# Kernel tuning notes

Measured on AMD Instinct MI355X. Metric: run time of the kernel, lower is better.

The kernel has to match this reference:

```python
import jax, jax.numpy as jnp
import numpy as np

C_M, C_Z, C_H = 256, 128, 32
N_SEQ, N_RES = 128, 256
EPS = 1e-3


def setup_inputs() -> dict:
    key = jax.random.key(0)
    ks = jax.random.split(key, 8)
    s = 0.02
    return {
        "m": jax.random.normal(ks[0], (N_SEQ, N_RES, C_M), dtype=jnp.float32),
        "mask": jnp.ones((N_SEQ, N_RES), dtype=jnp.float32),
        "ln_gamma": jnp.ones((C_M,), dtype=jnp.float32),
        "ln_beta": jnp.zeros((C_M,), dtype=jnp.float32),
        "W1": jax.random.normal(ks[1], (C_M, C_H), dtype=jnp.float32) * s,
        "b1": jnp.zeros((C_H,), dtype=jnp.float32),
        "W2": jax.random.normal(ks[2], (C_M, C_H), dtype=jnp.float32) * s,
        "b2": jnp.zeros((C_H,), dtype=jnp.float32),
        "Wout": jax.random.normal(ks[3], (C_H * C_H, C_Z), dtype=jnp.float32) * s,
        "bout": jnp.zeros((C_Z,), dtype=jnp.float32),
    }


def reference(m, mask, ln_gamma, ln_beta, W1, b1, W2, b2, Wout, bout):
    # LayerNorm over last dim (c_m)
    mu = jnp.mean(m, axis=-1, keepdims=True)
    var = jnp.var(m, axis=-1, keepdims=True)
    ln = (m - mu) * jax.lax.rsqrt(var + 1e-5) * ln_gamma + ln_beta

    mk = mask[..., None]                       # [S, R, 1]
    a = (ln @ W1 + b1) * mk                    # [S, R, c_h]
    b = (ln @ W2 + b2) * mk                    # [S, R, c_h]

    # outer-product mean: contract over the MSA seq dim
    outer = jnp.einsum('sbc,sde->bdce', a, b)  # [R, R, c_h, c_h]
    outer = outer.reshape(N_RES, N_RES, C_H * C_H)
    outer = outer @ Wout + bout                # [R, R, c_z]

    norm = jnp.einsum('sb,sd->bd', mask, mask)[..., None] + EPS  # [R, R, 1]
    return outer / norm
```

## Files before the change

kernel.cpp:

```cpp
#include <hip/hip_runtime.h>

#define S_DIM 128
#define R_DIM 256
#define CM 256
#define CH 32
#define CZ 128

typedef short bf16x8 __attribute__((ext_vector_type(8)));
typedef float f32x4 __attribute__((ext_vector_type(4)));
typedef unsigned short ushort_t;

static __device__ __forceinline__ unsigned short f2bf(float f) {
  union { float f; unsigned u; } v; v.f = f;
  unsigned r = v.u + 0x7FFF + ((v.u >> 16) & 1);
  return (unsigned short)(r >> 16);
}
static __device__ __forceinline__ float bf2f(unsigned short b) {
  union { unsigned u; float f; } v; v.u = ((unsigned)b) << 16;
  return v.f;
}

static __device__ __forceinline__ void gload_lds16(const void* g, void* l) {
  __builtin_amdgcn_global_load_lds(
      (const __attribute__((address_space(1))) void*)g,
      (__attribute__((address_space(3))) void*)l, 16, 0, 0);
}

__global__ __launch_bounds__(256) void prep_kernel(
    const float* __restrict__ W1, const float* __restrict__ b1,
    const float* __restrict__ W2, const float* __restrict__ b2,
    const float* __restrict__ gamma, const float* __restrict__ beta,
    ushort_t* __restrict__ pwT, float* __restrict__ SGCB) {
  int c = blockIdx.x;
  int cm = threadIdx.x;
  __shared__ float red[8];
  float w = (c < 32) ? W1[cm * 32 + c] : W2[cm * 32 + (c - 32)];
  unsigned short pw = f2bf(gamma[cm] * w);
  pwT[c * 256 + cm] = pw;
  float sg = bf2f(pw), cb = beta[cm] * w;
  for (int o = 32; o > 0; o >>= 1) {
    sg += __shfl_down(sg, o);
    cb += __shfl_down(cb, o);
  }
  if ((cm & 63) == 0) { red[cm >> 6] = sg; red[4 + (cm >> 6)] = cb; }
  __syncthreads();
  if (cm == 0) {
    float s = red[0] + red[1] + red[2] + red[3];
    float q = red[4] + red[5] + red[6] + red[7];
    SGCB[c] = s;
    SGCB[64 + c] = q + ((c < 32) ? b1[c] : b2[c - 32]);
  }
}

__global__ __launch_bounds__(256) void proj_kernel(
    const float* __restrict__ m, const float* __restrict__ mask,
    const ushort_t* __restrict__ pwT, const float* __restrict__ SGCB,
    const float* __restrict__ Wout,
    ushort_t* __restrict__ aB, ushort_t* __restrict__ bB,
    ushort_t* __restrict__ WT, float* __restrict__ normT) {
  extern __shared__ char pmem[];
  int blk = blockIdx.x;
  int t = threadIdx.x;

  if (blk >= 512) {
    if (blk < 544) {
      int e = blk - 512;
      float* wS = (float*)pmem;
#pragma unroll
      for (int i = 0; i < 16; ++i) {
        int idx = i * 256 + t;
        int cc = idx >> 7, z = idx & 127;
        wS[cc * 129 + z] = Wout[(size_t)(cc * 32 + e) * CZ + z];
      }
      __syncthreads();
#pragma unroll
      for (int i = 0; i < 16; ++i) {
        int idx = i * 256 + t;
        int z = idx >> 5, cc = idx & 31;
        WT[(size_t)z * 1024 + e * 32 + cc] = f2bf(wS[cc * 129 + z]);
      }
    } else {
      int b = blk - 544;
      float ps = 0.f;
      for (int s = 0; s < S_DIM; ++s)
        ps += mask[s * R_DIM + b] * mask[s * R_DIM + t];
      normT[(size_t)b * R_DIM + t] = 1.0f / (ps + 1e-3f);
    }
    return;
  }

  ushort_t* mhS = (ushort_t*)pmem;
  __shared__ float s1S[64], s2S[64], mkS[64];

  int r = blk >> 1, sh = blk & 1;

  {
    int s = t >> 2, q = t & 3;
    const float* src = m + ((size_t)((sh * 64 + s) * R_DIM + r)) * CM + q * 64;
    float s1 = 0.f, s2 = 0.f;
#pragma unroll
    for (int i = 0; i < 8; ++i) {
      float4 v0 = *(const float4*)(src + i * 8);
      float4 v1 = *(const float4*)(src + i * 8 + 4);
      float xs[8] = {v0.x, v0.y, v0.z, v0.w, v1.x, v1.y, v1.z, v1.w};
      union { ushort_t h[8]; float4 f; } H;
#pragma unroll
      for (int j = 0; j < 8; ++j) {
        float x = xs[j];
        s1 += x; s2 += x * x;
        H.h[j] = f2bf(x);
      }
      int ch = q * 8 + i, phys = ch ^ (s & 15);
      *(float4*)&mhS[s * 256 + phys * 8] = H.f;
    }
    s1 += __shfl_xor(s1, 1); s1 += __shfl_xor(s1, 2);
    s2 += __shfl_xor(s2, 1); s2 += __shfl_xor(s2, 2);
    if (q == 0) {
      s1S[s] = s1; s2S[s] = s2;
      mkS[s] = mask[(sh * 64 + s) * R_DIM + r];
    }
  }
  __syncthreads();

  int wave = t >> 6, lane = t & 63, l16 = lane & 15, lk = lane >> 4;
  int wm = wave >> 1, wn = wave & 1;
  f32x4 zero4 = {0.f, 0.f, 0.f, 0.f};
  f32x4 acc[2][2];
  acc[0][0] = zero4; acc[0][1] = zero4; acc[1][0] = zero4; acc[1][1] = zero4;

#pragma unroll
  for (int kstep = 0; kstep < 8; ++kstep) {
    int mm = kstep * 4 + lk;
    bf16x8 bw[2];
#pragma unroll
    for (int nf = 0; nf < 2; ++nf) {
      int cr = wn * 32 + nf * 16 + l16;
      bw[nf] = *(const bf16x8*)(pwT + cr * 256 + mm * 8);
    }
#pragma unroll
    for (int mf = 0; mf < 2; ++mf) {
      int srow = wm * 32 + mf * 16 + l16;
      int phys = mm ^ (srow & 15);
      bf16x8 ah = *(const bf16x8*)&mhS[srow * 256 + phys * 8];
#pragma unroll
      for (int nf = 0; nf < 2; ++nf)
        acc[mf][nf] = __builtin_amdgcn_mfma_f32_16x16x32_bf16(ah, bw[nf], acc[mf][nf], 0, 0, 0);
    }
  }

#pragma unroll
  for (int nf = 0; nf < 2; ++nf) {
    int c = wn * 32 + nf * 16 + l16;
    float sgv = SGCB[c], cbv = SGCB[64 + c];
#pragma unroll
    for (int mf = 0; mf < 2; ++mf) {
      union { ushort_t u[4]; uint2 v; } pk;
#pragma unroll
      for (int j = 0; j < 4; ++j) {
        int s = wm * 32 + mf * 16 + lk * 4 + j;
        float mu = s1S[s] * (1.0f / CM);
        float var = s2S[s] * (1.0f / CM) - mu * mu;
        float ri = rsqrtf(var + 1e-5f);
        float val = (ri * (acc[mf][nf][j] - mu * sgv) + cbv) * mkS[s];
        pk.u[j] = f2bf(val);
      }
      int sg0 = sh * 64 + wm * 32 + mf * 16 + lk * 4;
      if (c < 32)
        *(uint2*)&aB[((size_t)(r * 32 + c)) * S_DIM + sg0] = pk.v;
      else
        *(uint2*)&bB[((size_t)(r * 32 + (c - 32))) * S_DIM + sg0] = pk.v;
    }
  }
}

__global__ __launch_bounds__(512, 2) void outer_mfma_kernel(
    const ushort_t* __restrict__ aB, const ushort_t* __restrict__ bB,
    const ushort_t* __restrict__ WT, const float* __restrict__ normT,
    const float* __restrict__ bout, float* __restrict__ out) {
  extern __shared__ char smem[];
  __shared__ float nrm[64];
  int t = threadIdx.x;
  int lane = t & 63, wave = t >> 6;
  int l16 = lane & 15, lk = lane >> 4;

  int bid = blockIdx.x;
  int swz = (bid & 7) * 128 + (bid >> 3);
  int b0 = (swz >> 5) * 8, d0 = (swz & 31) * 8;

  {
    const ushort_t* srcA = aB + (size_t)b0 * 32 * S_DIM;
    const ushort_t* srcB = bB + (size_t)d0 * 32 * S_DIM;
#pragma unroll
    for (int i = 0; i < 16; ++i) {
      int cid = t + i * 512;
      int q = cid & 4095, row = q >> 4, pm = q & 15;
      int lg = pm ^ (row & 15);
      const ushort_t* src = (cid & 4096) ? srcB : srcA;
      gload_lds16(src + (size_t)row * S_DIM + lg * 8, smem + cid * 16);
    }
  }

  if (t < 64) nrm[t] = normT[(size_t)(b0 + (t >> 3)) * R_DIM + d0 + (t & 7)];

  __syncthreads();

  int wm = wave >> 1, wn = wave & 1;
  f32x4 zero4 = {0.f, 0.f, 0.f, 0.f};
  f32x4 acc[4][8];
#pragma unroll
  for (int i = 0; i < 4; ++i)
#pragma unroll
    for (int j = 0; j < 8; ++j) acc[i][j] = zero4;

#pragma unroll
  for (int ks = 0; ks < 4; ++ks) {
    int mm = ks * 4 + lk;
    bf16x8 af[4], bf[8];
#pragma unroll
    for (int r = 0; r < 4; ++r) {
      int row = wm * 64 + r * 16 + l16;
      af[r] = *(const bf16x8*)(smem + row * 256 + ((mm ^ (row & 15)) << 4));
    }
#pragma unroll
    for (int c = 0; c < 8; ++c) {
      int row = wn * 128 + c * 16 + l16;
      bf[c] = *(const bf16x8*)(smem + 65536 + row * 256 + ((mm ^ (row & 15)) << 4));
    }
#pragma unroll
    for (int r = 0; r < 4; ++r)
#pragma unroll
      for (int c = 0; c < 8; ++c)
        acc[r][c] = __builtin_amdgcn_mfma_f32_16x16x32_bf16(af[r], bf[c], acc[r][c], 0, 0, 0);
  }
  __syncthreads();

  int z = wave * 16 + l16;
  const ushort_t* wtz = WT + (size_t)z * 1024;
  bf16x8 wtb[8];
  wtb[0] = *(const bf16x8*)(wtz + lk * 8);
  wtb[1] = *(const bf16x8*)(wtz + 32 + lk * 8);
  wtb[2] = *(const bf16x8*)(wtz + 64 + lk * 8);
  wtb[3] = *(const bf16x8*)(wtz + 96 + lk * 8);

#define TSTORE(rr, cc_)                                                        \
  {                                                                            \
    int Mrow = wm * 64 + (rr) * 16 + lk * 4;                                   \
    int bsub = Mrow >> 5, cc = Mrow & 31;                                      \
    int Ncol = wn * 128 + (cc_) * 16 + l16;                                    \
    int dsub = Ncol >> 5, e = Ncol & 31;                                       \
    int p = bsub * 8 + dsub;                                                   \
    int chunk = e * 4 + (cc >> 3);                                             \
    int pch = chunk ^ ((chunk >> 3) & 7) ^ (p & 15);                           \
    union { ushort_t u[4]; uint2 v; } pk;                                      \
    pk.u[0] = f2bf(acc[rr][cc_][0]);                                           \
    pk.u[1] = f2bf(acc[rr][cc_][1]);                                           \
    pk.u[2] = f2bf(acc[rr][cc_][2]);                                           \
    pk.u[3] = f2bf(acc[rr][cc_][3]);                                           \
    *(uint2*)(smem + p * 2048 + pch * 16 + (cc & 4) * 2) = pk.v;               \
  }

#pragma unroll
  for (int r = 0; r < 4; ++r)
#pragma unroll
    for (int ci = 0; ci < 4; ++ci) TSTORE(r, ci * 2);
  __syncthreads();

#pragma unroll
  for (int r = 0; r < 4; ++r)
#pragma unroll
    for (int ci = 0; ci < 4; ++ci) TSTORE(r, ci * 2 + 1);
#undef TSTORE

#define ARD(ks, pf)                                                            \
  (*(const bf16x8*)(smem + ((pf) * 16 + l16) * 2048 +                          \
                    ((((ks) * 4 + lk) ^ ((((ks) * 4 + lk) >> 3) & 7) ^         \
                      (((pf) * 16 + l16) & 15))                                \
                     << 4)))

  f32x4 oc[4];
#pragma unroll
  for (int i = 0; i < 4; ++i) oc[i] = zero4;

  wtb[4] = *(const bf16x8*)(wtz + 128 + lk * 8);
  wtb[5] = *(const bf16x8*)(wtz + 160 + lk * 8);
  wtb[6] = *(const bf16x8*)(wtz + 192 + lk * 8);
  wtb[7] = *(const bf16x8*)(wtz + 224 + lk * 8);

  bf16x8 a_cur[4], a_nxt[4];
#pragma unroll
  for (int pf = 0; pf < 4; ++pf) a_cur[pf] = ARD(0, pf);

#pragma unroll
  for (int ks = 0; ks < 16; ++ks) {
    bf16x8 bfr = wtb[ks & 7];
    if (ks + 8 < 32)
      wtb[ks & 7] = *(const bf16x8*)(wtz + (ks + 8) * 32 + lk * 8);
    if (ks + 1 < 16) {
#pragma unroll
      for (int pf = 0; pf < 4; ++pf) a_nxt[pf] = ARD(ks + 1, pf);
    }
#pragma unroll
    for (int pf = 0; pf < 4; ++pf)
      oc[pf] = __builtin_amdgcn_mfma_f32_16x16x32_bf16(a_cur[pf], bfr, oc[pf], 0, 0, 0);
#pragma unroll
    for (int pf = 0; pf < 4; ++pf) a_cur[pf] = a_nxt[pf];
  }
  __syncthreads();

#pragma unroll
  for (int pf = 0; pf < 4; ++pf) a_cur[pf] = ARD(16, pf);
#pragma unroll
  for (int ks = 16; ks < 32; ++ks) {
    bf16x8 bfr = wtb[ks & 7];
    if (ks + 8 < 32)
      wtb[ks & 7] = *(const bf16x8*)(wtz + (ks + 8) * 32 + lk * 8);
    if (ks + 1 < 32) {
#pragma unroll
      for (int pf = 0; pf < 4; ++pf) a_nxt[pf] = ARD(ks + 1, pf);
    }
#pragma unroll
    for (int pf = 0; pf < 4; ++pf)
      oc[pf] = __builtin_amdgcn_mfma_f32_16x16x32_bf16(a_cur[pf], bfr, oc[pf], 0, 0, 0);
#pragma unroll
    for (int pf = 0; pf < 4; ++pf) a_cur[pf] = a_nxt[pf];
  }
#undef ARD

  float bo = bout[z];
#pragma unroll
  for (int pf = 0; pf < 4; ++pf) {
#pragma unroll
    for (int j = 0; j < 4; ++j) {
      int p = pf * 16 + lk * 4 + j;
      int b = b0 + (p >> 3), d = d0 + (p & 7);
      out[((size_t)(b * R_DIM + d)) * CZ + z] = (oc[pf][j] + bo) * nrm[p];
    }
  }
}

extern "C" void kernel_launch(void* const* d_in, const int* in_sizes, int n_in,
                              void* d_out, int out_size, void* d_ws, size_t ws_size,
                              hipStream_t stream) {
  const float* m     = (const float*)d_in[0];
  const float* mask  = (const float*)d_in[1];
  const float* gamma = (const float*)d_in[2];
  const float* beta  = (const float*)d_in[3];
  const float* W1    = (const float*)d_in[4];
  const float* b1    = (const float*)d_in[5];
  const float* W2    = (const float*)d_in[6];
  const float* b2    = (const float*)d_in[7];
  const float* Wout  = (const float*)d_in[8];
  const float* bout  = (const float*)d_in[9];
  float* out = (float*)d_out;

  char* ws = (char*)d_ws;
  ushort_t* aB    = (ushort_t*)ws;
  ushort_t* bB    = (ushort_t*)(ws + (size_t)2 * 1024 * 1024);
  ushort_t* WT    = (ushort_t*)(ws + (size_t)4 * 1024 * 1024);
  ushort_t* pwT   = (ushort_t*)(ws + (size_t)4352 * 1024);
  float*    SGCB  = (float*)   (ws + (size_t)4416 * 1024);
  float*    normT = (float*)   (ws + (size_t)4480 * 1024);

  hipFuncSetAttribute((const void*)outer_mfma_kernel,
                      hipFuncAttributeMaxDynamicSharedMemorySize, 131072);
  hipFuncSetAttribute((const void*)proj_kernel,
                      hipFuncAttributeMaxDynamicSharedMemorySize, 32768);

  prep_kernel<<<64, 256, 0, stream>>>(W1, b1, W2, b2, gamma, beta, pwT, SGCB);
  proj_kernel<<<800, 256, 32768, stream>>>(m, mask, pwT, SGCB, Wout,
                                           aB, bB, WT, normT);
  outer_mfma_kernel<<<1024, 512, 131072, stream>>>(aB, bB, WT, normT, bout, out);
}
```

Before: 78.01 us.

## Shrink outer-product tile to 4x4 residue pairs with more blocks and occupancy

Changes the fused outer-product kernel's tile from 8x8 to 4x4 residue pairs. Grid grows to 4096 blocks, dynamic LDS drops to 64KB, and launch bounds ask for 4 blocks per CU. The split LDS transpose phase and its extra barrier are removed, and the second GEMM uses two interleaved accumulators. The aim is more occupancy and latency hiding, but the smaller tile reloads each a/b row and the full Wout far more often, so global and L2 traffic per output rises.

```diff
diff --git a/kernel.cpp b/kernel.cpp
--- a/kernel.cpp
+++ b/kernel.cpp
@@ -173,63 +173,63 @@
   }
 }
 
-__global__ __launch_bounds__(512, 2) void outer_mfma_kernel(
+__global__ __launch_bounds__(512, 4) void outer_mfma_kernel(
     const ushort_t* __restrict__ aB, const ushort_t* __restrict__ bB,
     const ushort_t* __restrict__ WT, const float* __restrict__ normT,
     const float* __restrict__ bout, float* __restrict__ out) {
   extern __shared__ char smem[];
-  __shared__ float nrm[64];
+  __shared__ float nrm[16];
   int t = threadIdx.x;
   int lane = t & 63, wave = t >> 6;
   int l16 = lane & 15, lk = lane >> 4;
 
   int bid = blockIdx.x;
-  int swz = (bid & 7) * 128 + (bid >> 3);
-  int b0 = (swz >> 5) * 8, d0 = (swz & 31) * 8;
+  int swz = (bid & 7) * 512 + (bid >> 3);
+  int b0 = (swz >> 6) * 4, d0 = (swz & 63) * 4;
 
   {
     const ushort_t* srcA = aB + (size_t)b0 * 32 * S_DIM;
     const ushort_t* srcB = bB + (size_t)d0 * 32 * S_DIM;
 #pragma unroll
-    for (int i = 0; i < 16; ++i) {
+    for (int i = 0; i < 8; ++i) {
       int cid = t + i * 512;
-      int q = cid & 4095, row = q >> 4, pm = q & 15;
+      int q = cid & 2047, row = q >> 4, pm = q & 15;
       int lg = pm ^ (row & 15);
-      const ushort_t* src = (cid & 4096) ? srcB : srcA;
+      const ushort_t* src = (cid & 2048) ? srcB : srcA;
       gload_lds16(src + (size_t)row * S_DIM + lg * 8, smem + cid * 16);
     }
   }
 
-  if (t < 64) nrm[t] = normT[(size_t)(b0 + (t >> 3)) * R_DIM + d0 + (t & 7)];
-
-  __syncthreads();
-
-  int wm = wave >> 1, wn = wave & 1;
+  if (t < 16) nrm[t] = normT[(size_t)(b0 + (t >> 2)) * R_DIM + d0 + (t & 3)];
+
+  __syncthreads();
+
+  int wm = wave >> 2, wn = wave & 3;
   f32x4 zero4 = {0.f, 0.f, 0.f, 0.f};
-  f32x4 acc[4][8];
-#pragma unroll
-  for (int i = 0; i < 4; ++i)
-#pragma unroll
-    for (int j = 0; j < 8; ++j) acc[i][j] = zero4;
+  f32x4 acc[4][2];
+#pragma unroll
+  for (int i = 0; i < 4; ++i) {
+    acc[i][0] = zero4; acc[i][1] = zero4;
+  }
 
 #pragma unroll
   for (int ks = 0; ks < 4; ++ks) {
     int mm = ks * 4 + lk;
-    bf16x8 af[4], bf[8];
+    bf16x8 af[4], bf[2];
 #pragma unroll
     for (int r = 0; r < 4; ++r) {
       int row = wm * 64 + r * 16 + l16;
       af[r] = *(const bf16x8*)(smem + row * 256 + ((mm ^ (row & 15)) << 4));
     }
 #pragma unroll
-    for (int c = 0; c < 8; ++c) {
-      int row = wn * 128 + c * 16 + l16;
-      bf[c] = *(const bf16x8*)(smem + 65536 + row * 256 + ((mm ^ (row & 15)) << 4));
+    for (int c = 0; c < 2; ++c) {
+      int row = wn * 32 + c * 16 + l16;
+      bf[c] = *(const bf16x8*)(smem + 32768 + row * 256 + ((mm ^ (row & 15)) << 4));
     }
 #pragma unroll
     for (int r = 0; r < 4; ++r)
 #pragma unroll
-      for (int c = 0; c < 8; ++c)
+      for (int c = 0; c < 2; ++c)
         acc[r][c] = __builtin_amdgcn_mfma_f32_16x16x32_bf16(af[r], bf[c], acc[r][c], 0, 0, 0);
   }
   __syncthreads();
@@ -246,9 +246,9 @@
   {                                                                            \
     int Mrow = wm * 64 + (rr) * 16 + lk * 4;                                   \
     int bsub = Mrow >> 5, cc = Mrow & 31;                                      \
-    int Ncol = wn * 128 + (cc_) * 16 + l16;                                    \
+    int Ncol = wn * 32 + (cc_) * 16 + l16;                                     \
     int dsub = Ncol >> 5, e = Ncol & 31;                                       \
-    int p = bsub * 8 + dsub;                                                   \
+    int p = bsub * 4 + dsub;                                                   \
     int chunk = e * 4 + (cc >> 3);                                             \
     int pch = chunk ^ ((chunk >> 3) & 7) ^ (p & 15);                           \
     union { ushort_t u[4]; uint2 v; } pk;                                      \
@@ -262,79 +262,42 @@
 #pragma unroll
   for (int r = 0; r < 4; ++r)
 #pragma unroll
-    for (int ci = 0; ci < 4; ++ci) TSTORE(r, ci * 2);
-  __syncthreads();
-
-#pragma unroll
-  for (int r = 0; r < 4; ++r)
-#pragma unroll
-    for (int ci = 0; ci < 4; ++ci) TSTORE(r, ci * 2 + 1);
+    for (int ci = 0; ci < 2; ++ci) TSTORE(r, ci);
 #undef TSTORE
-
-#define ARD(ks, pf)                                                            \
-  (*(const bf16x8*)(smem + ((pf) * 16 + l16) * 2048 +                          \
-                    ((((ks) * 4 + lk) ^ ((((ks) * 4 + lk) >> 3) & 7) ^         \
-                      (((pf) * 16 + l16) & 15))                                \
+  __syncthreads();
+
+#define ARD(kk)                                                                \
+  (*(const bf16x8*)(smem + l16 * 2048 +                                        \
+                    ((((kk) * 4 + lk) ^ ((((kk) * 4 + lk) >> 3) & 7) ^         \
+                      (l16 & 15))                                              \
                      << 4)))
 
-  f32x4 oc[4];
-#pragma unroll
-  for (int i = 0; i < 4; ++i) oc[i] = zero4;
+  f32x4 oc[2];
+  oc[0] = zero4; oc[1] = zero4;
 
   wtb[4] = *(const bf16x8*)(wtz + 128 + lk * 8);
   wtb[5] = *(const bf16x8*)(wtz + 160 + lk * 8);
   wtb[6] = *(const bf16x8*)(wtz + 192 + lk * 8);
   wtb[7] = *(const bf16x8*)(wtz + 224 + lk * 8);
 
-  bf16x8 a_cur[4], a_nxt[4];
-#pragma unroll
-  for (int pf = 0; pf < 4; ++pf) a_cur[pf] = ARD(0, pf);
-
-#pragma unroll
-  for (int ks = 0; ks < 16; ++ks) {
+  bf16x8 a_cur = ARD(0), a_nxt;
+#pragma unroll
+  for (int ks = 0; ks < 32; ++ks) {
     bf16x8 bfr = wtb[ks & 7];
     if (ks + 8 < 32)
       wtb[ks & 7] = *(const bf16x8*)(wtz + (ks + 8) * 32 + lk * 8);
-    if (ks + 1 < 16) {
-#pragma unroll
-      for (int pf = 0; pf < 4; ++pf) a_nxt[pf] = ARD(ks + 1, pf);
-    }
-#pragma unroll
-    for (int pf = 0; pf < 4; ++pf)
-      oc[pf] = __builtin_amdgcn_mfma_f32_16x16x32_bf16(a_cur[pf], bfr, oc[pf], 0, 0, 0);
-#pragma unroll
-    for (int pf = 0; pf < 4; ++pf) a_cur[pf] = a_nxt[pf];
-  }
-  __syncthreads();
-
-#pragma unroll
-  for (int pf = 0; pf < 4; ++pf) a_cur[pf] = ARD(16, pf);
-#pragma unroll
-  for (int ks = 16; ks < 32; ++ks) {
-    bf16x8 bfr = wtb[ks & 7];
-    if (ks + 8 < 32)
-      wtb[ks & 7] = *(const bf16x8*)(wtz + (ks + 8) * 32 + lk * 8);
-    if (ks + 1 < 32) {
-#pragma unroll
-      for (int pf = 0; pf < 4; ++pf) a_nxt[pf] = ARD(ks + 1, pf);
-    }
-#pragma unroll
-    for (int pf = 0; pf < 4; ++pf)
-      oc[pf] = __builtin_amdgcn_mfma_f32_16x16x32_bf16(a_cur[pf], bfr, oc[pf], 0, 0, 0);
-#pragma unroll
-    for (int pf = 0; pf < 4; ++pf) a_cur[pf] = a_nxt[pf];
+    if (ks + 1 < 32) a_nxt = ARD(ks + 1);
+    oc[ks & 1] = __builtin_amdgcn_mfma_f32_16x16x32_bf16(a_cur, bfr, oc[ks & 1], 0, 0, 0);
+    a_cur = a_nxt;
   }
 #undef ARD
 
   float bo = bout[z];
 #pragma unroll
-  for (int pf = 0; pf < 4; ++pf) {
-#pragma unroll
-    for (int j = 0; j < 4; ++j) {
-      int p = pf * 16 + lk * 4 + j;
-      int b = b0 + (p >> 3), d = d0 + (p & 7);
-      out[((size_t)(b * R_DIM + d)) * CZ + z] = (oc[pf][j] + bo) * nrm[p];
-    }
+  for (int j = 0; j < 4; ++j) {
+    int p = lk * 4 + j;
+    int b = b0 + (p >> 2), d = d0 + (p & 3);
+    out[((size_t)(b * R_DIM + d)) * CZ + z] = (oc[0][j] + oc[1][j] + bo) * nrm[p];
   }
 }
 
@@ -362,12 +325,12 @@
   float*    normT = (float*)   (ws + (size_t)4480 * 1024);
 
   hipFuncSetAttribute((const void*)outer_mfma_kernel,
-                      hipFuncAttributeMaxDynamicSharedMemorySize, 131072);
+                      hipFuncAttributeMaxDynamicSharedMemorySize, 65536);
   hipFuncSetAttribute((const void*)proj_kernel,
                       hipFuncAttributeMaxDynamicSharedMemorySize, 32768);
 
   prep_kernel<<<64, 256, 0, stream>>>(W1, b1, W2, b2, gamma, beta, pwT, SGCB);
   proj_kernel<<<800, 256, 32768, stream>>>(m, mask, pwT, SGCB, Wout,
                                            aB, bB, WT, normT);
-  outer_mfma_kernel<<<1024, 512, 131072, stream>>>(aB, bB, WT, normT, bout, out);
-}
+  outer_mfma_kernel<<<4096, 512, 65536, stream>>>(aB, bB, WT, normT, bout, out);
+}
```

Measured after the change: 152.2 us. 95.1% more time.
